# Performance work log

Measured on AMD Instinct MI355X. Metric: run time of the kernel, lower is better.

## Reference

```python
import jax, jax.numpy as jnp
import numpy as np

B, S, D, H = 2, 4096, 512, 8
HD = D // H  # head_dim = 64


def setup_inputs() -> dict:
    key = jax.random.key(0)
    ks = jax.random.split(key, 7)
    scale = 1.0 / np.sqrt(D)
    return {
        "x": jax.random.normal(ks[0], (B, S, D), dtype=jnp.float32),
        "Wq": jax.random.uniform(ks[1], (D, D), jnp.float32, -scale, scale),
        "bq": jax.random.uniform(ks[2], (D,), jnp.float32, -scale, scale),
        "Wk": jax.random.uniform(ks[3], (D, D), jnp.float32, -scale, scale),
        "bk": jax.random.uniform(ks[4], (D,), jnp.float32, -scale, scale),
        "Wv": jax.random.uniform(ks[5], (D, D), jnp.float32, -scale, scale),
        "bv": jax.random.uniform(ks[6], (D,), jnp.float32, -scale, scale),
    }


def reference(x, Wq, bq, Wk, bk, Wv, bv):
    # torch Linear: y = x @ W.T + b
    q = x @ Wq.T + bq  # [B,S,D]
    k = x @ Wk.T + bk
    v = x @ Wv.T + bv
    # split heads -> [B,H,S,HD]
    q = q.reshape(B, S, H, HD).transpose(0, 2, 1, 3)
    k = k.reshape(B, S, H, HD).transpose(0, 2, 1, 3)
    v = v.reshape(B, S, H, HD).transpose(0, 2, 1, 3)
    # NOTE: module scales by sqrt(pitch_dim), NOT sqrt(head_dim) -- keep faithful.
    scores = jnp.einsum("bhqd,bhkd->bhqk", q, k) / jnp.sqrt(jnp.float32(D))
    causal = jnp.tril(jnp.ones((S, S), dtype=bool))  # lower-tri incl. diag allowed
    scores = jnp.where(causal, scores, -jnp.inf)
    attn = jax.nn.softmax(scores, axis=-1)
    out = jnp.einsum("bhqk,bhkd->bhqd", attn, v)  # [B,H,S,HD]
    return out.transpose(0, 2, 1, 3).reshape(B, S, D)
```

## Files before the change

kernel.cpp:

```cpp
#include <hip/hip_runtime.h>
#include <hip/hip_bf16.h>
#include <math.h>

#define BB 2
#define SS 4096
#define DD 512
#define HH 8
#define HD 64
#define MSD (BB*SS*DD)
#define WSZ (DD*DD)

#define XOFF (4*(size_t)MSD)
#define WOFF (5*(size_t)MSD)
#define POFF (3*(size_t)MSD)

typedef __attribute__((ext_vector_type(8))) short bf16x8;
typedef __attribute__((ext_vector_type(4))) float f32x4;

__device__ __forceinline__ unsigned short f2bf(float f) {
    unsigned int u = __float_as_uint(f);
    u += 0x7fff + ((u >> 16) & 1);
    return (unsigned short)(u >> 16);
}
__device__ __forceinline__ unsigned int pk2bf(float a, float b) {
    __hip_bfloat162 h = __float22bfloat162_rn(make_float2(a, b));
    union { __hip_bfloat162 h2; unsigned int u; } cv; cv.h2 = h;
    return cv.u;
}

#define GLD16(gsrc, ldst) \
    __builtin_amdgcn_global_load_lds((const __attribute__((address_space(1))) unsigned int*)(gsrc), \
                                     (__attribute__((address_space(3))) unsigned int*)(ldst), 16, 0, 0)

#define CH(qb,t0,t1) ((unsigned)(qb) | ((unsigned)(t0)<<8) | ((unsigned)(t1)<<16))
__device__ __constant__ unsigned int SCHED[48] = {
  CH(31,0,32),  CH(31,32,64), CH(0,0,2),
  CH(15,0,32),  CH(29,0,30),  CH(1,0,4),
  CH(29,30,60), CH(14,0,30),  CH(2,0,6),
  CH(28,0,29),  CH(28,29,58), CH(3,0,8),
  CH(27,0,28),  CH(13,0,28),  CH(4,0,10),
  CH(26,0,27),  CH(26,27,54), CH(5,0,12),
  CH(25,0,26),  CH(12,0,26),  CH(6,0,14),
  CH(24,0,25),  CH(24,25,50), CH(7,0,16),
  CH(30,0,31),  CH(17,0,18),  CH(16,0,17),
  CH(30,31,62), CH(17,18,36), CH(16,17,34),
  CH(27,28,56), CH(19,0,20),  CH(8,0,18),
  CH(25,26,52), CH(20,0,21),  CH(18,0,19),
  CH(23,0,24),  CH(22,0,23),  CH(18,19,38),
  CH(23,24,48), CH(21,0,22),  CH(19,20,40),
  CH(11,0,24),  CH(21,22,44), CH(9,0,20),
  CH(22,23,46), CH(10,0,22),  CH(20,21,42),
};

__global__ __launch_bounds__(256)
void convert_bf16(const float* __restrict__ x,
                  const float* __restrict__ Wq, const float* __restrict__ Wk,
                  const float* __restrict__ Wv, unsigned short* __restrict__ ws) {
    const int i8 = blockIdx.x*256 + threadIdx.x;
    const float* src; unsigned short* dst; size_t off;
    if (i8 < MSD/8) {
        src = x; dst = ws + XOFF; off = (size_t)i8 * 8;
    } else {
        size_t o = ((size_t)i8 - MSD/8) * 8;
        int wsel = (int)(o / WSZ);
        src = (wsel == 0) ? Wq : (wsel == 1) ? Wk : Wv;
        dst = ws + WOFF + (size_t)wsel*WSZ;
        off = o % WSZ;
    }
    float4 a = *(const float4*)&src[off];
    float4 b = *(const float4*)&src[off+4];
    unsigned short r[8] = { f2bf(a.x), f2bf(a.y), f2bf(a.z), f2bf(a.w),
                            f2bf(b.x), f2bf(b.y), f2bf(b.z), f2bf(b.w) };
    *(bf16x8*)&dst[off] = *(const bf16x8*)r;
}

__global__ __launch_bounds__(512, 2)
void qkv_fused(const float* __restrict__ bq, const float* __restrict__ bk,
               const float* __restrict__ bv, unsigned short* __restrict__ ws) {
    const unsigned short* Xb = ws + XOFF;
    const unsigned short* Wz0 = ws + WOFF;
    const unsigned short* Wz1 = ws + WOFF + WSZ;
    const unsigned short* Wz2 = ws + WOFF + 2*(size_t)WSZ;

    __shared__ __align__(16) unsigned short As[2][128*64];
    __shared__ __align__(16) unsigned short Bs[3][2][128*64];

    const int tid  = threadIdx.x;
    const int w    = tid >> 6, l = tid & 63;
    const int quad = l >> 4,  r16 = l & 15;
    const int wm   = w >> 2,  wn  = w & 3;
    const int n0   = blockIdx.x * 128;
    const int m0   = blockIdx.y * 128;

    const int sr8 = l >> 3, sc = l & 7;

    f32x4 acc[3][4][2];
    #pragma unroll
    for (int z = 0; z < 3; ++z)
        #pragma unroll
        for (int i = 0; i < 4; ++i)
            #pragma unroll
            for (int j = 0; j < 2; ++j) acc[z][i][j] = (f32x4){0.f,0.f,0.f,0.f};

    auto STAGE = [&](int k0, int b) {
        #pragma unroll
        for (int u = 0; u < 2; ++u) {
            const int r0  = w*16 + u*8;
            const int row = r0 + sr8;
            const int c   = sc ^ (row & 7);
            GLD16(&Xb [(size_t)(m0 + row)*DD + k0 + c*8], &As[b][r0*64]);
            GLD16(&Wz0[(size_t)(n0 + row)*DD + k0 + c*8], &Bs[0][b][r0*64]);
            GLD16(&Wz1[(size_t)(n0 + row)*DD + k0 + c*8], &Bs[1][b][r0*64]);
            GLD16(&Wz2[(size_t)(n0 + row)*DD + k0 + c*8], &Bs[2][b][r0*64]);
        }
    };

    STAGE(0, 0);

    #pragma unroll
    for (int kt = 0; kt < 8; ++kt) {
        __syncthreads();
        if (kt + 1 < 8) STAGE((kt + 1)*64, (kt + 1) & 1);

        const int bb = kt & 1;
        #pragma unroll
        for (int kc = 0; kc < 2; ++kc) {
            bf16x8 a[4];
            #pragma unroll
            for (int i = 0; i < 4; ++i) {
                const int mr = wm*64 + i*16 + r16;
                a[i] = *(const bf16x8*)&As[bb][mr*64 + (((kc*4+quad) ^ (mr&7))*8)];
            }
            bf16x8 b0[2], b1[2], b2[2];
            #pragma unroll
            for (int j = 0; j < 2; ++j) {
                const int nr = wn*32 + j*16 + r16;
                const int sw = ((kc*4+quad) ^ (nr&7))*8;
                b0[j] = *(const bf16x8*)&Bs[0][bb][nr*64 + sw];
                b1[j] = *(const bf16x8*)&Bs[1][bb][nr*64 + sw];
                b2[j] = *(const bf16x8*)&Bs[2][bb][nr*64 + sw];
            }
            __builtin_amdgcn_s_setprio(1);
            #pragma unroll
            for (int i = 0; i < 4; ++i)
                #pragma unroll
                for (int j = 0; j < 2; ++j) {
                    acc[0][i][j] = __builtin_amdgcn_mfma_f32_16x16x32_bf16(b0[j], a[i], acc[0][i][j], 0, 0, 0);
                    acc[1][i][j] = __builtin_amdgcn_mfma_f32_16x16x32_bf16(b1[j], a[i], acc[1][i][j], 0, 0, 0);
                    acc[2][i][j] = __builtin_amdgcn_mfma_f32_16x16x32_bf16(a[i], b2[j], acc[2][i][j], 0, 0, 0);
                }
            __builtin_amdgcn_s_setprio(0);
        }
    }

    __syncthreads();
    unsigned short* Ct = &As[0][0];
    const float qscale = 0.04419417382415922f * 1.4426950408889634f;
    const float* biases[3] = { bq, bk, bv };

    #pragma unroll
    for (int z = 0; z < 3; ++z) {
        unsigned short* dst = ws + (size_t)z*MSD;
        const float* bias = biases[z];

        if (z == 2) {
            #pragma unroll
            for (int j = 0; j < 2; ++j) {
                const int nloc = wn*32 + j*16 + r16;
                const float bz = bias[n0 + nloc];
                #pragma unroll
                for (int i = 0; i < 4; ++i) {
                    const int chunk = wm*8 + i*2 + (quad>>1);
                    const int off   = (quad & 1) * 4;
                    unsigned short r4[4];
                    #pragma unroll
                    for (int reg = 0; reg < 4; ++reg)
                        r4[reg] = f2bf(acc[2][i][j][reg] + bz);
                    *(uint2*)&Ct[nloc*128 + ((chunk ^ (nloc & 7))*8) + off] = *(const uint2*)r4;
                }
            }
        } else {
            #pragma unroll
            for (int j = 0; j < 2; ++j) {
                const int nbase = wn*32 + j*16 + quad*4;
                const float4 bz4 = *(const float4*)&bias[n0 + nbase];
                const int chunk = wn*4 + j*2 + (quad>>1);
                const int off   = (quad & 1) * 4;
                #pragma unroll
                for (int i = 0; i < 4; ++i) {
                    const int mloc = wm*64 + i*16 + r16;
                    float v0 = acc[z][i][j][0] + bz4.x;
                    float v1 = acc[z][i][j][1] + bz4.y;
                    float v2 = acc[z][i][j][2] + bz4.z;
                    float v3 = acc[z][i][j][3] + bz4.w;
                    if (z == 0) { v0 *= qscale; v1 *= qscale; v2 *= qscale; v3 *= qscale; }
                    unsigned short r4[4] = { f2bf(v0), f2bf(v1), f2bf(v2), f2bf(v3) };
                    *(uint2*)&Ct[mloc*128 + ((chunk ^ (mloc & 7))*8) + off] = *(const uint2*)r4;
                }
            }
        }
        __syncthreads();

        if (z == 2) {
            const int b_ = m0 >> 12, s0_ = m0 & (SS-1);
            #pragma unroll
            for (int p = 0; p < 4; ++p) {
                const int f = p*512 + tid;
                const int nrow = f >> 4;
                const int mch  = f & 15;
                bf16x8 v = *(const bf16x8*)&Ct[nrow*128 + ((mch ^ (nrow & 7))*8)];
                const int ng = n0 + nrow;
                const int h = ng >> 6, hd = ng & 63;
                *(bf16x8*)&dst[((size_t)(b_*HH + h)*HD + hd)*SS + s0_ + mch*8] = v;
            }
        } else {
            #pragma unroll
            for (int p = 0; p < 4; ++p) {
                const int f = p*512 + tid;
                const int hh  = f >> 10;
                const int rem = f & 1023;
                const int sr  = rem >> 3;
                const int ch  = rem & 7;
                bf16x8 v = *(const bf16x8*)&Ct[sr*128 + (((hh*8 + ch) ^ (sr & 7))*8)];
                const int mg = m0 + sr;
                const int b_ = mg >> 12, s_ = mg & (SS-1);
                const int hg = (n0 >> 6) + hh;
                *(bf16x8*)&dst[((size_t)(b_*HH + hg)*SS + s_)*HD + ch*8] = v;
            }
        }
        if (z < 2) __syncthreads();
    }
}

__global__ __launch_bounds__(256, 4)
void attn_mfma(unsigned short* __restrict__ ws, float* __restrict__ out) {
    const int bx = blockIdx.x;
    const int k_ = bx >> 8;
    const int j_ = bx & 255;
    const int bh = j_ & 15;
    const int ti = j_ >> 4;
    const unsigned int e = SCHED[ti*3 + k_];
    const int qb = e & 255;
    const int t0 = (e >> 8) & 255;
    const int t1 = (e >> 16) & 255;
    const int split = !(t0 == 0 && t1 == 2*qb + 2);
    const int half  = (t0 != 0);

    const int tid  = threadIdx.x;
    const int w    = tid >> 6, l = tid & 63;
    const int quad = l >> 4,  r16 = l & 15;
    const int qlo  = qb*128 + w*32;
    const int tdiag = 2*qb + (w >> 1);
    const int qoff  = 32*(w & 1);

    const unsigned short* Qg  = ws;
    const unsigned short* Kg  = ws + (size_t)MSD;
    const unsigned short* Vtg = ws + 2*(size_t)MSD;

    __shared__ __align__(16) unsigned short Ks[2][64*64];
    __shared__ __align__(16) unsigned short Vs[2][64*64];

    const size_t kbase = (size_t)bh*SS*HD;
    const size_t vbase = (size_t)bh*HD*SS;

    bf16x8 bqf[2][2];
    #pragma unroll
    for (int nt = 0; nt < 2; ++nt)
        #pragma unroll
        for (int kc = 0; kc < 2; ++kc)
            bqf[nt][kc] = *(const bf16x8*)&Qg[kbase + (size_t)(qlo + nt*16 + r16)*HD + kc*32 + quad*8];

    const f32x4 ZZ = (f32x4){0.f,0.f,0.f,0.f};
    const unsigned short onep[8] = {0x3F80,0x3F80,0x3F80,0x3F80,0x3F80,0x3F80,0x3F80,0x3F80};
    const bf16x8 ones8 = *(const bf16x8*)onep;

    f32x4 od[4][2];
    #pragma unroll
    for (int mt = 0; mt < 4; ++mt)
        #pragma unroll
        for (int nt = 0; nt < 2; ++nt) od[mt][nt] = ZZ;
    f32x4 lacc[2] = {ZZ, ZZ};

    const int x7 = r16 & 7;
    const unsigned short* pK0 = &Ks[0][r16*64 + ((quad     ^ x7)*8)];
    const unsigned short* pK1 = &Ks[0][r16*64 + (((4+quad) ^ x7)*8)];
    const unsigned short* pV0 = &Vs[0][r16*64 + ((quad     ^ x7)*8)];
    const unsigned short* pV1 = &Vs[0][r16*64 + (((4+quad) ^ x7)*8)];

    const int sr8 = l >> 3, sc = l & 7;
    const int row0 = w*16 + sr8,     row1 = w*16 + 8 + sr8;
    const int c0   = sc ^ (row0 & 7), c1  = sc ^ (row1 & 7);
    const unsigned short* kg0 = Kg  + kbase + (size_t)(t0*64 + row0)*HD + c0*8;
    const unsigned short* kg1 = Kg  + kbase + (size_t)(t0*64 + row1)*HD + c1*8;
    const unsigned short* vg0 = Vtg + vbase + (size_t)row0*SS + t0*64 + c0*8;
    const unsigned short* vg1 = Vtg + vbase + (size_t)row1*SS + t0*64 + c1*8;
    unsigned short* lk0 = &Ks[0][(w*16    )*64];
    unsigned short* lk1 = &Ks[0][(w*16 + 8)*64];
    unsigned short* lv0 = &Vs[0][(w*16    )*64];
    unsigned short* lv1 = &Vs[0][(w*16 + 8)*64];

    GLD16(kg0, lk0); GLD16(kg1, lk1);
    GLD16(vg0, lv0); GLD16(vg1, lv1);
    kg0 += 64*HD; kg1 += 64*HD; vg0 += 64; vg1 += 64;

    for (int t = t0; t < t1; ++t) {
        __syncthreads();

        if (t + 1 < t1) {
            const int d1 = ((t + 1 - t0) & 1) * 4096;
            GLD16(kg0, lk0 + d1); GLD16(kg1, lk1 + d1);
            GLD16(vg0, lv0 + d1); GLD16(vg1, lv1 + d1);
            kg0 += 64*HD; kg1 += 64*HD; vg0 += 64; vg1 += 64;
        }

        if (t <= tdiag) {
            const int boff = ((t - t0) & 1) * 4096;

            f32x4 z[4][2];
            __builtin_amdgcn_s_setprio(1);
            #pragma unroll
            for (int mt = 0; mt < 4; ++mt) {
                bf16x8 ak0 = *(const bf16x8*)(pK0 + boff + mt*1024);
                bf16x8 ak1 = *(const bf16x8*)(pK1 + boff + mt*1024);
                #pragma unroll
                for (int nt = 0; nt < 2; ++nt) {
                    z[mt][nt] = __builtin_amdgcn_mfma_f32_16x16x32_bf16(ak0, bqf[nt][0], ZZ, 0, 0, 0);
                    z[mt][nt] = __builtin_amdgcn_mfma_f32_16x16x32_bf16(ak1, bqf[nt][1], z[mt][nt], 0, 0, 0);
                }
            }
            __builtin_amdgcn_s_setprio(0);

            if (t == tdiag) {
                #pragma unroll
                for (int mt = 0; mt < 4; ++mt)
                    #pragma unroll
                    for (int nt = 0; nt < 2; ++nt)
                        #pragma unroll
                        for (int reg = 0; reg < 4; ++reg)
                            if (mt*16 + quad*4 + reg > qoff + nt*16 + r16)
                                z[mt][nt][reg] = -1e30f;
            }

            unsigned int X0[4][2], X1[4][2];
            #pragma unroll
            for (int mt = 0; mt < 4; ++mt)
                #pragma unroll
                for (int nt = 0; nt < 2; ++nt) {
                    X0[mt][nt] = pk2bf(__builtin_amdgcn_exp2f(z[mt][nt][0]),
                                       __builtin_amdgcn_exp2f(z[mt][nt][1]));
                    X1[mt][nt] = pk2bf(__builtin_amdgcn_exp2f(z[mt][nt][2]),
                                       __builtin_amdgcn_exp2f(z[mt][nt][3]));
                }

            bf16x8 pf[2][2];
            #pragma unroll
            for (int nt = 0; nt < 2; ++nt)
                #pragma unroll
                for (int kc = 0; kc < 2; ++kc) {
                    unsigned int a0 = X0[2*kc][nt], b0 = X0[2*kc+1][nt];
                    unsigned int a1 = X1[2*kc][nt], b1 = X1[2*kc+1][nt];
                    asm("v_permlane32_swap_b32 %0, %1" : "+v"(a0), "+v"(b0));
                    asm("v_permlane16_swap_b32 %0, %1" : "+v"(a0), "+v"(b0));
                    asm("v_permlane32_swap_b32 %0, %1" : "+v"(a1), "+v"(b1));
                    asm("v_permlane16_swap_b32 %0, %1" : "+v"(a1), "+v"(b1));
                    unsigned int wv[4] = { a0, a1, b0, b1 };
                    pf[nt][kc] = *(const bf16x8*)wv;
                }

            __builtin_amdgcn_s_setprio(1);
            #pragma unroll
            for (int nt = 0; nt < 2; ++nt) {
                lacc[nt] = __builtin_amdgcn_mfma_f32_16x16x32_bf16(ones8, pf[nt][0], lacc[nt], 0, 0, 0);
                lacc[nt] = __builtin_amdgcn_mfma_f32_16x16x32_bf16(ones8, pf[nt][1], lacc[nt], 0, 0, 0);
            }
            #pragma unroll
            for (int mt = 0; mt < 4; ++mt) {
                bf16x8 av0 = *(const bf16x8*)(pV0 + boff + mt*1024);
                bf16x8 av1 = *(const bf16x8*)(pV1 + boff + mt*1024);
                #pragma unroll
                for (int nt = 0; nt < 2; ++nt) {
                    od[mt][nt] = __builtin_amdgcn_mfma_f32_16x16x32_bf16(av0, pf[nt][0], od[mt][nt], 0, 0, 0);
                    od[mt][nt] = __builtin_amdgcn_mfma_f32_16x16x32_bf16(av1, pf[nt][1], od[mt][nt], 0, 0, 0);
                }
            }
            __builtin_amdgcn_s_setprio(0);
        }
    }

    if (split) {
        const int p = 2*(bh*16 + (qb - 16)) + half;
        float* Op = (float*)(ws + POFF) + (size_t)p*(128*64);
        float* Lp = (float*)(ws + WOFF) + p*128;
        #pragma unroll
        for (int nt = 0; nt < 2; ++nt) {
            const int qloc = w*32 + nt*16 + r16;
            if (quad == 0) Lp[qloc] = lacc[nt][0];
            #pragma unroll
            for (int mt = 0; mt < 4; ++mt)
                *(f32x4*)&Op[(size_t)qloc*64 + mt*16 + quad*4] = od[mt][nt];
        }
    } else {
        const int b_ = bh >> 3, h = bh & 7;
        #pragma unroll
        for (int nt = 0; nt < 2; ++nt) {
            const float inv = 1.0f / lacc[nt][0];
            const int q = qlo + nt*16 + r16;
            float* op = out + ((size_t)(b_*SS + q))*DD + h*HD;
            #pragma unroll
            for (int mt = 0; mt < 4; ++mt) {
                float4 tt;
                tt.x = od[mt][nt][0]*inv; tt.y = od[mt][nt][1]*inv;
                tt.z = od[mt][nt][2]*inv; tt.w = od[mt][nt][3]*inv;
                *(float4*)&op[mt*16 + quad*4] = tt;
            }
        }
    }
}

__global__ __launch_bounds__(256)
void attn_combine(const unsigned short* __restrict__ ws, float* __restrict__ out) {
    const int i  = blockIdx.x*256 + threadIdx.x;
    const int d4 = i & 15;
    const int q  = (i >> 4) & 127;
    const int r  = i >> 11;
    const int bh = r >> 4, qb = 16 + (r & 15);

    const float* Opart = (const float*)(ws + POFF);
    const float* Lpart = (const float*)(ws + WOFF);

    const float4 a = *(const float4*)&Opart[((size_t)(2*r)*128 + q)*64 + d4*4];
    const float4 b = *(const float4*)&Opart[((size_t)(2*r + 1)*128 + q)*64 + d4*4];
    const float lt = Lpart[(2*r)*128 + q] + Lpart[(2*r + 1)*128 + q];
    const float inv = 1.0f / lt;

    const int qg = qb*128 + q;
    const int b_ = bh >> 3, h = bh & 7;
    float4 o;
    o.x = (a.x + b.x)*inv; o.y = (a.y + b.y)*inv;
    o.z = (a.z + b.z)*inv; o.w = (a.w + b.w)*inv;
    *(float4*)&out[((size_t)(b_*SS + qg))*DD + h*HD + d4*4] = o;
}

extern "C" void kernel_launch(void* const* d_in, const int* in_sizes, int n_in,
                              void* d_out, int out_size, void* d_ws, size_t ws_size,
                              hipStream_t stream) {
    const float* x  = (const float*)d_in[0];
    const float* Wq = (const float*)d_in[1];
    const float* bq = (const float*)d_in[2];
    const float* Wk = (const float*)d_in[3];
    const float* bk = (const float*)d_in[4];
    const float* Wv = (const float*)d_in[5];
    const float* bv = (const float*)d_in[6];
    float* out = (float*)d_out;
    unsigned short* ws = (unsigned short*)d_ws;

    const int nconv = (MSD/8 + 3*WSZ/8 + 255) / 256;
    convert_bf16<<<nconv, 256, 0, stream>>>(x, Wq, Wk, Wv, ws);

    dim3 ggrid(DD/128, (BB*SS)/128);
    qkv_fused<<<ggrid, 512, 0, stream>>>(bq, bk, bv, ws);

    attn_mfma<<<768, 256, 0, stream>>>(ws, out);
    attn_combine<<<2048, 256, 0, stream>>>(ws, out);
}
```

Before: 152.3 us.

## Fuse x fp32-to-bf16 conversion into QKV GEMM staging

The standalone conversion of x to bf16 is removed. The QKV GEMM now loads fp32 x directly into registers, converts it, and writes it into swizzled LDS, so the bf16 copy of x no longer makes a round trip through global memory. Only the weights are still converted in a separate small kernel. The cost is an extra __syncthreads per k-step, and x is read four times, once per n-block, at twice the byte size, with register-prefetched loads in place of async global-to-LDS loads.

```diff
diff --git a/kernel.cpp b/kernel.cpp
--- a/kernel.cpp
+++ b/kernel.cpp
@@ -10,7 +10,6 @@
 #define MSD (BB*SS*DD)
 #define WSZ (DD*DD)
 
-#define XOFF (4*(size_t)MSD)
 #define WOFF (5*(size_t)MSD)
 #define POFF (3*(size_t)MSD)
 
@@ -26,6 +25,11 @@
     __hip_bfloat162 h = __float22bfloat162_rn(make_float2(a, b));
     union { __hip_bfloat162 h2; unsigned int u; } cv; cv.h2 = h;
     return cv.u;
+}
+__device__ __forceinline__ bf16x8 cvt8(const float4& a, const float4& b) {
+    unsigned int wv[4] = { pk2bf(a.x, a.y), pk2bf(a.z, a.w),
+                           pk2bf(b.x, b.y), pk2bf(b.z, b.w) };
+    return *(const bf16x8*)wv;
 }
 
 #define GLD16(gsrc, ldst) \
@@ -53,31 +57,23 @@
 };
 
 __global__ __launch_bounds__(256)
-void convert_bf16(const float* __restrict__ x,
-                  const float* __restrict__ Wq, const float* __restrict__ Wk,
-                  const float* __restrict__ Wv, unsigned short* __restrict__ ws) {
+void convert_w(const float* __restrict__ Wq, const float* __restrict__ Wk,
+               const float* __restrict__ Wv, unsigned short* __restrict__ ws) {
     const int i8 = blockIdx.x*256 + threadIdx.x;
-    const float* src; unsigned short* dst; size_t off;
-    if (i8 < MSD/8) {
-        src = x; dst = ws + XOFF; off = (size_t)i8 * 8;
-    } else {
-        size_t o = ((size_t)i8 - MSD/8) * 8;
-        int wsel = (int)(o / WSZ);
-        src = (wsel == 0) ? Wq : (wsel == 1) ? Wk : Wv;
-        dst = ws + WOFF + (size_t)wsel*WSZ;
-        off = o % WSZ;
-    }
+    size_t o = (size_t)i8 * 8;
+    const int wsel = (int)(o / WSZ);
+    const float* src = (wsel == 0) ? Wq : (wsel == 1) ? Wk : Wv;
+    unsigned short* dst = ws + WOFF + (size_t)wsel*WSZ;
+    const size_t off = o % WSZ;
     float4 a = *(const float4*)&src[off];
     float4 b = *(const float4*)&src[off+4];
-    unsigned short r[8] = { f2bf(a.x), f2bf(a.y), f2bf(a.z), f2bf(a.w),
-                            f2bf(b.x), f2bf(b.y), f2bf(b.z), f2bf(b.w) };
-    *(bf16x8*)&dst[off] = *(const bf16x8*)r;
+    *(bf16x8*)&dst[off] = cvt8(a, b);
 }
 
 __global__ __launch_bounds__(512, 2)
-void qkv_fused(const float* __restrict__ bq, const float* __restrict__ bk,
+void qkv_fused(const float* __restrict__ x,
+               const float* __restrict__ bq, const float* __restrict__ bk,
                const float* __restrict__ bv, unsigned short* __restrict__ ws) {
-    const unsigned short* Xb = ws + XOFF;
     const unsigned short* Wz0 = ws + WOFF;
     const unsigned short* Wz1 = ws + WOFF + WSZ;
     const unsigned short* Wz2 = ws + WOFF + 2*(size_t)WSZ;
@@ -102,27 +98,48 @@
             #pragma unroll
             for (int j = 0; j < 2; ++j) acc[z][i][j] = (f32x4){0.f,0.f,0.f,0.f};
 
-    auto STAGE = [&](int k0, int b) {
+    const int arow0 = w*16 +     sr8;
+    const int arow1 = w*16 + 8 + sr8;
+    const float* xa0 = x + (size_t)(m0 + arow0)*DD + (sc ^ (arow0 & 7))*8;
+    const float* xa1 = x + (size_t)(m0 + arow1)*DD + (sc ^ (arow1 & 7))*8;
+    unsigned short* da0[2] = { &As[0][arow0*64 + sc*8], &As[1][arow0*64 + sc*8] };
+    unsigned short* da1[2] = { &As[0][arow1*64 + sc*8], &As[1][arow1*64 + sc*8] };
+
+    auto STAGE_B = [&](int k0, int b) {
         #pragma unroll
         for (int u = 0; u < 2; ++u) {
             const int r0  = w*16 + u*8;
             const int row = r0 + sr8;
             const int c   = sc ^ (row & 7);
-            GLD16(&Xb [(size_t)(m0 + row)*DD + k0 + c*8], &As[b][r0*64]);
             GLD16(&Wz0[(size_t)(n0 + row)*DD + k0 + c*8], &Bs[0][b][r0*64]);
             GLD16(&Wz1[(size_t)(n0 + row)*DD + k0 + c*8], &Bs[1][b][r0*64]);
             GLD16(&Wz2[(size_t)(n0 + row)*DD + k0 + c*8], &Bs[2][b][r0*64]);
         }
     };
 
-    STAGE(0, 0);
+    STAGE_B(0, 0);
+    float4 ra[4];
+    ra[0] = *(const float4*)xa0; ra[1] = *(const float4*)(xa0+4);
+    ra[2] = *(const float4*)xa1; ra[3] = *(const float4*)(xa1+4);
+    xa0 += 64; xa1 += 64;
 
     #pragma unroll
     for (int kt = 0; kt < 8; ++kt) {
         __syncthreads();
-        if (kt + 1 < 8) STAGE((kt + 1)*64, (kt + 1) & 1);
 
         const int bb = kt & 1;
+        *(bf16x8*)da0[bb] = cvt8(ra[0], ra[1]);
+        *(bf16x8*)da1[bb] = cvt8(ra[2], ra[3]);
+
+        __syncthreads();
+
+        if (kt + 1 < 8) {
+            STAGE_B((kt + 1)*64, (kt + 1) & 1);
+            ra[0] = *(const float4*)xa0; ra[1] = *(const float4*)(xa0+4);
+            ra[2] = *(const float4*)xa1; ra[3] = *(const float4*)(xa1+4);
+            xa0 += 64; xa1 += 64;
+        }
+
         #pragma unroll
         for (int kc = 0; kc < 2; ++kc) {
             bf16x8 a[4];
@@ -454,11 +471,10 @@
     float* out = (float*)d_out;
     unsigned short* ws = (unsigned short*)d_ws;
 
-    const int nconv = (MSD/8 + 3*WSZ/8 + 255) / 256;
-    convert_bf16<<<nconv, 256, 0, stream>>>(x, Wq, Wk, Wv, ws);
+    convert_w<<<384, 256, 0, stream>>>(Wq, Wk, Wv, ws);
 
     dim3 ggrid(DD/128, (BB*SS)/128);
-    qkv_fused<<<ggrid, 512, 0, stream>>>(bq, bk, bv, ws);
+    qkv_fused<<<ggrid, 512, 0, stream>>>(x, bq, bk, bv, ws);
 
     attn_mfma<<<768, 256, 0, stream>>>(ws, out);
     attn_combine<<<2048, 256, 0, stream>>>(ws, out);
```

After: 151.9 us. Within noise of the previous version (-0.3%).
